# Kernel tuning notes

Hardware: AMD Instinct MI355X
Metric: run time of the kernel (lower is better)

## Reference

```python
import jax, jax.numpy as jnp
import numpy as np

L, B, H, D, P, T = 3, 64, 1024, 128, 64, 512  # layers, batch, hidden, input_dim, prompt, timesteps


def setup_inputs() -> dict:
    key = jax.random.key(0)
    ks = jax.random.split(key, 20)
    s = 1.0 / np.sqrt(H)  # PyTorch LSTM/Linear init scale
    u = lambda k, shape: jax.random.uniform(k, shape, jnp.float32, -s, s)
    inp = {
        "x": jax.random.uniform(ks[0], (P, B, D), jnp.float32),
        "h0": jax.random.normal(ks[1], (L, B, H), jnp.float32),
        "c0": jax.random.normal(ks[2], (L, B, H), jnp.float32),
        "W_ih0": u(ks[3], (4 * H, D)),
        "W_hh0": u(ks[4], (4 * H, H)),
        "b_ih0": u(ks[5], (4 * H,)),
        "b_hh0": u(ks[6], (4 * H,)),
        "W_ih1": u(ks[7], (4 * H, H)),
        "W_hh1": u(ks[8], (4 * H, H)),
        "b_ih1": u(ks[9], (4 * H,)),
        "b_hh1": u(ks[10], (4 * H,)),
        "W_ih2": u(ks[11], (4 * H, H)),
        "W_hh2": u(ks[12], (4 * H, H)),
        "b_ih2": u(ks[13], (4 * H,)),
        "b_hh2": u(ks[14], (4 * H,)),
        "W_fc": u(ks[15], (D, H)),
        "b_fc": u(ks[16], (D,)),
        "timesteps": T,
    }
    return inp


def _lstm_cell(inp, h, c, W_ih, W_hh, b):
    # PyTorch gate order: i, f, g, o
    gates = inp @ W_ih.T + h @ W_hh.T + b  # (B, 4H)
    i, f, g, o = jnp.split(gates, 4, axis=-1)
    c_new = jax.nn.sigmoid(f) * c + jax.nn.sigmoid(i) * jnp.tanh(g)
    h_new = jax.nn.sigmoid(o) * jnp.tanh(c_new)
    return h_new, c_new


def reference(x, h0, c0, W_ih0, W_hh0, b_ih0, b_hh0, W_ih1, W_hh1, b_ih1, b_hh1,
              W_ih2, W_hh2, b_ih2, b_hh2, W_fc, b_fc, timesteps):
    Tn = int(timesteps)
    Pn = x.shape[0]
    layers = [
        (W_ih0, W_hh0, b_ih0 + b_hh0),
        (W_ih1, W_hh1, b_ih1 + b_hh1),
        (W_ih2, W_hh2, b_ih2 + b_hh2),
    ]
    # teacher-forcing inputs padded to full horizon
    x_pad = jnp.zeros((Tn,) + x.shape[1:], x.dtype).at[:Pn].set(x)

    def step(carry, t):
        net_in, h, c = carry  # net_in (B,D); h,c (L,B,H)
        layer_in = net_in
        hs, cs = [], []
        for l, (Wi, Wh, b) in enumerate(layers):
            hl, cl = _lstm_cell(layer_in, h[l], c[l], Wi, Wh, b)
            hs.append(hl)
            cs.append(cl)
            layer_in = hl
        gen = jax.nn.sigmoid(layer_in @ W_fc.T + b_fc)  # (B, D)
        nxt = jnp.where(t + 1 < Pn, x_pad[t + 1], gen)
        return (nxt, jnp.stack(hs), jnp.stack(cs)), nxt

    init = (x[0], h0, c0)
    _, emitted = jax.lax.scan(step, init, jnp.arange(Tn - 1))  # (T-1, B, D)
    out = jnp.concatenate([x[:1], emitted], axis=0)  # (T, B, D)
    return out
```

## Files before the change

### kernel.cpp

```cpp
#include <hip/hip_runtime.h>

typedef short v8s __attribute__((ext_vector_type(8)));
typedef float f32x4 __attribute__((ext_vector_type(4)));
typedef unsigned short u16;

static constexpr int kB = 64;
static constexpr int kH = 1024;
static constexpr int kD = 128;
static constexpr int kL = 3;
static constexpr int NBLK = 128;
static constexpr int NTHR = 512;
static constexpr int NFLAG = 16384;

__device__ __forceinline__ u16 f2b(float f) {
  union { float f; unsigned u; } v; v.f = f;
  unsigned r = v.u + 0x7fffu + ((v.u >> 16) & 1u);
  return (u16)(r >> 16);
}

__device__ __forceinline__ float sigm(float x) { return 1.f / (1.f + expf(-x)); }

__device__ __forceinline__ void st16(u16* p, u16 v) {
  unsigned d = v;
  asm volatile("global_store_short %0, %1, off sc0 sc1" :: "v"(p), "v"(d) : "memory");
}
__device__ __forceinline__ void st32(float* p, float v) {
  asm volatile("global_store_dword %0, %1, off sc0 sc1" :: "v"(p), "v"(v) : "memory");
}
__device__ __forceinline__ void st32u(unsigned* p, unsigned v) {
  asm volatile("global_store_dword %0, %1, off sc0 sc1" :: "v"(p), "v"(v) : "memory");
}

__device__ __forceinline__ void ld4cv(v8s& a0, v8s& a1, v8s& a2, v8s& a3,
                                      const u16* p0, const u16* p1,
                                      const u16* p2, const u16* p3) {
  asm volatile(
      "global_load_dwordx4 %0, %4, off sc0 sc1\n\t"
      "global_load_dwordx4 %1, %5, off sc0 sc1\n\t"
      "global_load_dwordx4 %2, %6, off sc0 sc1\n\t"
      "global_load_dwordx4 %3, %7, off sc0 sc1"
      : "=&v"(a0), "=&v"(a1), "=&v"(a2), "=&v"(a3)
      : "v"(p0), "v"(p1), "v"(p2), "v"(p3)
      : "memory");
}
#define WAITV(N) do { asm volatile("s_waitcnt vmcnt(" #N ")" ::: "memory"); \
                      __builtin_amdgcn_sched_barrier(0); } while (0)
#define MFMA8(A, W, I, ACC) do { \
  _Pragma("unroll") \
  for (int mt_ = 0; mt_ < 4; ++mt_) { \
    ACC[0][mt_] = __builtin_amdgcn_mfma_f32_16x16x32_bf16(A[mt_], W[0][I], ACC[0][mt_], 0, 0, 0); \
    ACC[1][mt_] = __builtin_amdgcn_mfma_f32_16x16x32_bf16(A[mt_], W[1][I], ACC[1][mt_], 0, 0, 0); \
  } } while (0)

struct Params {
  const float *x, *h0, *c0;
  const float *Wi0, *Wh0, *bi0, *bh0;
  const float *Wi1, *Wh1, *bi1, *bh1;
  const float *Wi2, *Wh2, *bi2, *bh2;
  const float *Wfc, *bfc;
  float *out;
  u16 *wb0i, *wb0h, *wb1i, *wb1h, *wb2i, *wb2h, *wbfc;
  u16 *xb, *hA, *hB, *curx;
  float *b0, *b1, *b2, *bfcs;
  unsigned *bflags;
  int P, T;
};

__global__ void init_kernel(Params p) {
  long gid = (long)blockIdx.x * blockDim.x + threadIdx.x;
  long stride = (long)gridDim.x * blockDim.x;
  const long nw0i = 4096L * kD, nwh = 4096L * kH, nfc = (long)kD * kH;
  for (long i = gid; i < nw0i; i += stride) p.wb0i[i] = f2b(p.Wi0[i]);
  for (long i = gid; i < nwh; i += stride) {
    p.wb0h[i] = f2b(p.Wh0[i]);
    p.wb1i[i] = f2b(p.Wi1[i]);
    p.wb1h[i] = f2b(p.Wh1[i]);
    p.wb2i[i] = f2b(p.Wi2[i]);
    p.wb2h[i] = f2b(p.Wh2[i]);
  }
  for (long i = gid; i < nfc; i += stride) p.wbfc[i] = f2b(p.Wfc[i]);
  for (long i = gid; i < 4096; i += stride) {
    p.b0[i] = p.bi0[i] + p.bh0[i];
    p.b1[i] = p.bi1[i] + p.bh1[i];
    p.b2[i] = p.bi2[i] + p.bh2[i];
  }
  for (long i = gid; i < kD; i += stride) p.bfcs[i] = p.bfc[i];
  for (long i = gid; i < NFLAG; i += stride) p.bflags[i] = 0u;
  long nx = (long)p.P * kB * kD;
  for (long i = gid; i < nx; i += stride) {
    p.xb[i] = f2b(p.x[i]);
    p.out[i] = p.x[i];
  }
  long nh = (long)kL * kB * kH;
  for (long i = gid; i < nh; i += stride) p.hA[i] = f2b(p.h0[i]);
}

__global__ void __launch_bounds__(NTHR) rnn_kernel(Params p) {
  const int tid = threadIdx.x, bid = blockIdx.x;
  const int lane = tid & 63, w = tid >> 6;
  const int colc = lane & 15, kq = lane >> 4;
  const int aoff = kq * 8;
  const int u7 = colc & 7, gh = colc >> 3;
  const long wr0 = (long)gh * kH + bid * 8 + u7;
  const long wr1 = (long)(2 + gh) * kH + bid * 8 + u7;
  unsigned* f0arr = p.bflags;
  unsigned* f1arr = p.bflags + NBLK * 32;
  unsigned* f2arr = p.bflags + 2 * NBLK * 32;
  unsigned* xflag = p.bflags + 3 * NBLK * 32;

  v8s w0x[2];
  v8s w0h[2][4], w1x[2][4], w1h[2][4], w2x[2][4], w2h[2][4];
  if (w < 4) {
    w0x[0] = *(const v8s*)(p.wb0i + wr0 * kD + w * 32 + aoff);
    w0x[1] = *(const v8s*)(p.wb0i + wr1 * kD + w * 32 + aoff);
  }
#pragma unroll
  for (int i = 0; i < 4; ++i) {
    int k = (w + 8 * i) * 32 + aoff;
    w0h[0][i] = *(const v8s*)(p.wb0h + wr0 * kH + k);
    w0h[1][i] = *(const v8s*)(p.wb0h + wr1 * kH + k);
    w1x[0][i] = *(const v8s*)(p.wb1i + wr0 * kH + k);
    w1x[1][i] = *(const v8s*)(p.wb1i + wr1 * kH + k);
    w1h[0][i] = *(const v8s*)(p.wb1h + wr0 * kH + k);
    w1h[1][i] = *(const v8s*)(p.wb1h + wr1 * kH + k);
    w2x[0][i] = *(const v8s*)(p.wb2i + wr0 * kH + k);
    w2x[1][i] = *(const v8s*)(p.wb2i + wr1 * kH + k);
    w2h[0][i] = *(const v8s*)(p.wb2h + wr0 * kH + k);
    w2h[1][i] = *(const v8s*)(p.wb2h + wr1 * kH + k);
  }

  const int em = tid >> 3, eu = tid & 7;
  const int ehid = bid * 8 + eu;
  float cst[kL], brg[kL][4];
#pragma unroll
  for (int l = 0; l < kL; ++l)
    cst[l] = p.c0[(long)l * kB * kH + (long)em * kH + ehid];
  {
    const float* bp[3] = {p.b0, p.b1, p.b2};
#pragma unroll
    for (int l = 0; l < 3; ++l)
#pragma unroll
      for (int gg = 0; gg < 4; ++gg) brg[l][gg] = bp[l][gg * kH + ehid];
  }

  __shared__ float lg[8][64][18];
  const int T = p.T, P = p.P;
  const f32x4 z4 = {0.f, 0.f, 0.f, 0.f};

  auto epilogue = [&](int l, f32x4(&acc)[2][4], u16* hOut) {
    float pre[4];
#pragma unroll
    for (int mt = 0; mt < 4; ++mt)
#pragma unroll
      for (int r = 0; r < 4; ++r) lg[w][mt * 16 + kq * 4 + r][colc] = acc[0][mt][r];
    __syncthreads();
    {
      float s0 = 0.f, s1 = 0.f;
#pragma unroll
      for (int ww = 0; ww < 8; ++ww) {
        s0 += lg[ww][em][eu];
        s1 += lg[ww][em][8 + eu];
      }
      pre[0] = s0;
      pre[1] = s1;
    }
    __syncthreads();
#pragma unroll
    for (int mt = 0; mt < 4; ++mt)
#pragma unroll
      for (int r = 0; r < 4; ++r) lg[w][mt * 16 + kq * 4 + r][colc] = acc[1][mt][r];
    __syncthreads();
    {
      float s0 = 0.f, s1 = 0.f;
#pragma unroll
      for (int ww = 0; ww < 8; ++ww) {
        s0 += lg[ww][em][eu];
        s1 += lg[ww][em][8 + eu];
      }
      pre[2] = s0;
      pre[3] = s1;
    }
    float iv = pre[0] + brg[l][0], fv = pre[1] + brg[l][1];
    float gv = pre[2] + brg[l][2], ov = pre[3] + brg[l][3];
    float cn = sigm(fv) * cst[l] + sigm(iv) * tanhf(gv);
    cst[l] = cn;
    st16(hOut + (long)em * kH + ehid, f2b(sigm(ov) * tanhf(cn)));
  };

  auto arrive = [&](unsigned* farr, unsigned val) {
    asm volatile("s_waitcnt vmcnt(0)" ::: "memory");
    __syncthreads();
    if (tid == 0) st32u(farr + bid * 32, val);
  };

  auto poll16 = [&](unsigned* farr, unsigned tgt) {
    unsigned* fp = farr + (4 * (w + 8 * (lane >> 2)) + (lane & 3)) * 32;
    for (;;) {
      unsigned v = (lane < 16)
          ? __hip_atomic_load(fp, __ATOMIC_RELAXED, __HIP_MEMORY_SCOPE_AGENT)
          : tgt;
      if (__all((int)(v >= tgt))) break;
      __builtin_amdgcn_s_sleep(1);
    }
    asm volatile("" ::: "memory");
  };

  auto gemm16 = [&](const u16* Ab, v8s (&W)[2][4], f32x4 (&acc)[2][4]) {
    const u16* b0 = Ab + (long)colc * kH + w * 32 + aoff;
    const u16* b1 = b0 + 16 * kH;
    const u16* b2 = b0 + 32 * kH;
    const u16* b3 = b0 + 48 * kH;
    v8s A0[4], A1[4], A2[4], A3[4];
    ld4cv(A0[0], A0[1], A0[2], A0[3], b0, b1, b2, b3);
    ld4cv(A1[0], A1[1], A1[2], A1[3], b0 + 256, b1 + 256, b2 + 256, b3 + 256);
    WAITV(4);
    MFMA8(A0, W, 0, acc);
    ld4cv(A2[0], A2[1], A2[2], A2[3], b0 + 512, b1 + 512, b2 + 512, b3 + 512);
    WAITV(4);
    MFMA8(A1, W, 1, acc);
    ld4cv(A3[0], A3[1], A3[2], A3[3], b0 + 768, b1 + 768, b2 + 768, b3 + 768);
    WAITV(4);
    MFMA8(A2, W, 2, acc);
    WAITV(0);
    MFMA8(A3, W, 3, acc);
  };

  for (int t = 0; t < T - 1; ++t) {
    const u16* hOld = (t & 1) ? p.hB : p.hA;
    u16* hNew = (t & 1) ? p.hA : p.hB;
    const bool genstep = (t >= P);
    const unsigned ft = (unsigned)(t + 1);

    {
      f32x4 acc[2][4] = {z4, z4, z4, z4, z4, z4, z4, z4};
      if (genstep && bid < 8 && w < 4) {
        const unsigned t2 = (unsigned)t;
        unsigned* fa = f2arr + lane * 32;
        unsigned* fb = f2arr + (64 + lane) * 32;
        for (;;) {
          unsigned a = __hip_atomic_load(fa, __ATOMIC_RELAXED, __HIP_MEMORY_SCOPE_AGENT);
          unsigned b = __hip_atomic_load(fb, __ATOMIC_RELAXED, __HIP_MEMORY_SCOPE_AGENT);
          if (__all((int)((a >= t2) & (b >= t2)))) break;
          __builtin_amdgcn_s_sleep(1);
        }
        (void)__hip_atomic_load(f2arr, __ATOMIC_ACQUIRE, __HIP_MEMORY_SCOPE_AGENT);
        f32x4 u0 = z4, u1 = z4;
        const u16* ap = hOld + 2L * kB * kH + (long)(w * 16 + colc) * kH + aoff;
        const u16* bp = p.wbfc + (long)(bid * 16 + colc) * kH + aoff;
#pragma unroll
        for (int i = 0; i < 16; ++i) {
          v8s a0 = *(const v8s*)(ap + i * 32);
          v8s b0 = *(const v8s*)(bp + i * 32);
          v8s a1 = *(const v8s*)(ap + 512 + i * 32);
          v8s b1 = *(const v8s*)(bp + 512 + i * 32);
          u0 = __builtin_amdgcn_mfma_f32_16x16x32_bf16(a0, b0, u0, 0, 0, 0);
          u1 = __builtin_amdgcn_mfma_f32_16x16x32_bf16(a1, b1, u1, 0, 0, 0);
        }
        float bv = p.bfcs[bid * 16 + colc];
#pragma unroll
        for (int r = 0; r < 4; ++r) {
          float val = sigm(u0[r] + u1[r] + bv);
          int bb = w * 16 + kq * 4 + r, d = bid * 16 + colc;
          st32(p.out + (long)t * (kB * kD) + (long)bb * kD + d, val);
          st16(p.curx + (long)bb * kD + d, f2b(val));
        }
        asm volatile("s_waitcnt vmcnt(0)" ::: "memory");
        if (lane == 0)
          st32u(xflag + (bid * 4 + w) * 32, (unsigned)(t - P + 1));
      }
      gemm16(hOld, w0h, acc);
      if (w < 4) {
        if (genstep) {
          const unsigned tag = (unsigned)(t - P + 1);
          unsigned* fp = xflag + ((2 * w + (lane >> 2)) * 4 + (lane & 3)) * 32;
          for (;;) {
            unsigned v = (lane < 8)
                ? __hip_atomic_load(fp, __ATOMIC_RELAXED, __HIP_MEMORY_SCOPE_AGENT)
                : tag;
            if (__all((int)(v >= tag))) break;
            __builtin_amdgcn_s_sleep(1);
          }
          asm volatile("" ::: "memory");
          const u16* xb0 = p.curx + (long)colc * kD + w * 32 + aoff;
          v8s X[4];
          ld4cv(X[0], X[1], X[2], X[3],
                xb0, xb0 + 16 * kD, xb0 + 32 * kD, xb0 + 48 * kD);
          WAITV(0);
#pragma unroll
          for (int mt = 0; mt < 4; ++mt) {
            acc[0][mt] = __builtin_amdgcn_mfma_f32_16x16x32_bf16(X[mt], w0x[0], acc[0][mt], 0, 0, 0);
            acc[1][mt] = __builtin_amdgcn_mfma_f32_16x16x32_bf16(X[mt], w0x[1], acc[1][mt], 0, 0, 0);
          }
        } else {
          const u16* xin = p.xb + (long)t * kB * kD;
          int k = w * 32 + aoff;
#pragma unroll
          for (int mt = 0; mt < 4; ++mt) {
            v8s a = *(const v8s*)(xin + (long)(mt * 16 + colc) * kD + k);
            acc[0][mt] = __builtin_amdgcn_mfma_f32_16x16x32_bf16(a, w0x[0], acc[0][mt], 0, 0, 0);
            acc[1][mt] = __builtin_amdgcn_mfma_f32_16x16x32_bf16(a, w0x[1], acc[1][mt], 0, 0, 0);
          }
        }
      }
      epilogue(0, acc, hNew);
      arrive(f0arr, ft);
    }

    {
      f32x4 acc[2][4] = {z4, z4, z4, z4, z4, z4, z4, z4};
      gemm16(hOld + (long)kB * kH, w1h, acc);
      poll16(f0arr, ft);
      gemm16(hNew, w1x, acc);
      epilogue(1, acc, hNew + (long)kB * kH);
      arrive(f1arr, ft);
    }

    {
      f32x4 acc[2][4] = {z4, z4, z4, z4, z4, z4, z4, z4};
      gemm16(hOld + 2L * kB * kH, w2h, acc);
      poll16(f1arr, ft);
      gemm16(hNew + (long)kB * kH, w2x, acc);
      epilogue(2, acc, hNew + 2L * kB * kH);
      arrive(f2arr, ft);
    }
  }

  if (bid == 0 && T - 1 >= P && T >= 2) {
    const unsigned tgt = (unsigned)(T - 1);
    {
      const int i = threadIdx.x;
      unsigned* fp = f2arr + i * 32;
      for (;;) {
        unsigned v = (i < NBLK)
            ? __hip_atomic_load(fp, __ATOMIC_RELAXED, __HIP_MEMORY_SCOPE_AGENT)
            : tgt;
        if (__syncthreads_and((int)(v >= tgt))) break;
        __builtin_amdgcn_s_sleep(1);
      }
      if (tid == 0)
        (void)__hip_atomic_load(f2arr, __ATOMIC_ACQUIRE, __HIP_MEMORY_SCOPE_AGENT);
      __syncthreads();
    }
    const u16* hL = ((T - 2) & 1) ? p.hA : p.hB;
    const u16* wfc_r = p.wbfc + (long)(w * 16 + colc) * kH + aoff;
    const u16* ap = hL + 2L * kB * kH + (long)colc * kH + aoff;
    f32x4 fa[4] = {z4, z4, z4, z4};
#pragma unroll 2
    for (int kk = 0; kk < 32; ++kk) {
      v8s b = *(const v8s*)(wfc_r + kk * 32);
#pragma unroll
      for (int mt = 0; mt < 4; ++mt) {
        v8s a = *(const v8s*)(ap + mt * 16 * kH + kk * 32);
        fa[mt] = __builtin_amdgcn_mfma_f32_16x16x32_bf16(a, b, fa[mt], 0, 0, 0);
      }
    }
    float bv = p.bfcs[w * 16 + colc];
    float* orow = p.out + (long)(T - 1) * (kB * kD);
#pragma unroll
    for (int mt = 0; mt < 4; ++mt)
#pragma unroll
      for (int r = 0; r < 4; ++r) {
        int bb = mt * 16 + kq * 4 + r, d = w * 16 + colc;
        st32(orow + (long)bb * kD + d, sigm(fa[mt][r] + bv));
      }
  }
}

extern "C" void kernel_launch(void* const* d_in, const int* in_sizes, int n_in,
                              void* d_out, int out_size, void* d_ws, size_t ws_size,
                              hipStream_t stream) {
  Params p;
  p.x   = (const float*)d_in[0];
  p.h0  = (const float*)d_in[1];
  p.c0  = (const float*)d_in[2];
  p.Wi0 = (const float*)d_in[3];
  p.Wh0 = (const float*)d_in[4];
  p.bi0 = (const float*)d_in[5];
  p.bh0 = (const float*)d_in[6];
  p.Wi1 = (const float*)d_in[7];
  p.Wh1 = (const float*)d_in[8];
  p.bi1 = (const float*)d_in[9];
  p.bh1 = (const float*)d_in[10];
  p.Wi2 = (const float*)d_in[11];
  p.Wh2 = (const float*)d_in[12];
  p.bi2 = (const float*)d_in[13];
  p.bh2 = (const float*)d_in[14];
  p.Wfc = (const float*)d_in[15];
  p.bfc = (const float*)d_in[16];
  p.out = (float*)d_out;
  p.P = in_sizes[0] / (kB * kD);
  p.T = out_size / (kB * kD);

  char* w = (char*)d_ws;
  auto alloc = [&](size_t bytes) {
    char* r = w;
    w += (bytes + 255) & ~(size_t)255;
    return r;
  };
  p.wb0i = (u16*)alloc(4096L * kD * 2);
  p.wb0h = (u16*)alloc(4096L * kH * 2);
  p.wb1i = (u16*)alloc(4096L * kH * 2);
  p.wb1h = (u16*)alloc(4096L * kH * 2);
  p.wb2i = (u16*)alloc(4096L * kH * 2);
  p.wb2h = (u16*)alloc(4096L * kH * 2);
  p.wbfc = (u16*)alloc((long)kD * kH * 2);
  p.xb   = (u16*)alloc((long)p.P * kB * kD * 2);
  p.hA   = (u16*)alloc((long)kL * kB * kH * 2);
  p.hB   = (u16*)alloc((long)kL * kB * kH * 2);
  p.curx = (u16*)alloc((long)kB * kD * 2);
  p.b0   = (float*)alloc(4096 * 4);
  p.b1   = (float*)alloc(4096 * 4);
  p.b2   = (float*)alloc(4096 * 4);
  p.bfcs = (float*)alloc(kD * 4);
  p.bflags = (unsigned*)alloc(NFLAG * 4);

  hipLaunchKernelGGL(init_kernel, dim3(512), dim3(256), 0, stream, p);
  void* args[] = { &p };
  hipLaunchCooperativeKernel((const void*)rnn_kernel, dim3(NBLK), dim3(NTHR),
                             args, 0, stream);
}
```

Baseline: 19.54 ms.

## Offload FC head to dedicated blocks and merge epilogue LDS reductions

Adds eight extra cooperative blocks that compute only the output FC projection during generation steps, taking that work off the critical path of the first eight LSTM blocks. The FC blocks split the K dimension across two wave halves, reduce the halves through shared memory, and load their inputs with pipelined loads. The gate epilogue now stages both accumulator halves in one double-size LDS buffer, removing two barriers per layer. It also packs h outputs through LDS into 128-bit stores instead of scattered 16-bit stores. The launch bound now requests two blocks per CU, which could constrain register use for the register-resident weights.

```diff
diff --git a/kernel.cpp b/kernel.cpp
--- a/kernel.cpp
+++ b/kernel.cpp
@@ -9,6 +9,8 @@
 static constexpr int kD = 128;
 static constexpr int kL = 3;
 static constexpr int NBLK = 128;
+static constexpr int NFC = 8;
+static constexpr int NBLK_TOT = NBLK + NFC;
 static constexpr int NTHR = 512;
 static constexpr int NFLAG = 16384;
 
@@ -29,6 +31,9 @@
 }
 __device__ __forceinline__ void st32u(unsigned* p, unsigned v) {
   asm volatile("global_store_dword %0, %1, off sc0 sc1" :: "v"(p), "v"(v) : "memory");
+}
+__device__ __forceinline__ void st128(u16* p, v8s v) {
+  asm volatile("global_store_dwordx4 %0, %1, off sc0 sc1" :: "v"(p), "v"(v) : "memory");
 }
 
 __device__ __forceinline__ void ld4cv(v8s& a0, v8s& a1, v8s& a2, v8s& a3,
@@ -95,18 +100,85 @@
   for (long i = gid; i < nh; i += stride) p.hA[i] = f2b(p.h0[i]);
 }
 
-__global__ void __launch_bounds__(NTHR) rnn_kernel(Params p) {
+__global__ void __launch_bounds__(NTHR, 2) rnn_kernel(Params p) {
   const int tid = threadIdx.x, bid = blockIdx.x;
   const int lane = tid & 63, w = tid >> 6;
   const int colc = lane & 15, kq = lane >> 4;
   const int aoff = kq * 8;
-  const int u7 = colc & 7, gh = colc >> 3;
-  const long wr0 = (long)gh * kH + bid * 8 + u7;
-  const long wr1 = (long)(2 + gh) * kH + bid * 8 + u7;
   unsigned* f0arr = p.bflags;
   unsigned* f1arr = p.bflags + NBLK * 32;
   unsigned* f2arr = p.bflags + 2 * NBLK * 32;
   unsigned* xflag = p.bflags + 3 * NBLK * 32;
+  const int T = p.T, P = p.P;
+  const f32x4 z4 = {0.f, 0.f, 0.f, 0.f};
+
+  if (bid >= NBLK) {
+    if (T - 1 <= P) return;
+    __shared__ float fcred[4][64][4];
+    const int fbid = bid - NBLK;
+    const int wm = w & 3;
+    const int half = w >> 2;
+    const u16* bp = p.wbfc + (long)(fbid * 16 + colc) * kH + half * 512 + aoff;
+    const float bv = p.bfcs[fbid * 16 + colc];
+    for (int t = P; t < T - 1; ++t) {
+      const u16* hOld = (t & 1) ? p.hB : p.hA;
+      {
+        const unsigned tgt = (unsigned)t;
+        unsigned* fp = f2arr + (half * 64 + lane) * 32;
+        for (;;) {
+          unsigned v = __hip_atomic_load(fp, __ATOMIC_RELAXED, __HIP_MEMORY_SCOPE_AGENT);
+          if (__all((int)(v >= tgt))) break;
+          __builtin_amdgcn_s_sleep(1);
+        }
+        asm volatile("" ::: "memory");
+      }
+      const u16* ap = hOld + 2L * kB * kH + (long)(wm * 16 + colc) * kH + half * 512 + aoff;
+      f32x4 u = z4;
+      v8s A0[4], A1[4];
+      ld4cv(A0[0], A0[1], A0[2], A0[3], ap, ap + 32, ap + 64, ap + 96);
+      ld4cv(A1[0], A1[1], A1[2], A1[3], ap + 128, ap + 160, ap + 192, ap + 224);
+      WAITV(4);
+#pragma unroll
+      for (int j = 0; j < 4; ++j)
+        u = __builtin_amdgcn_mfma_f32_16x16x32_bf16(A0[j], *(const v8s*)(bp + j * 32), u, 0, 0, 0);
+      ld4cv(A0[0], A0[1], A0[2], A0[3], ap + 256, ap + 288, ap + 320, ap + 352);
+      WAITV(4);
+#pragma unroll
+      for (int j = 0; j < 4; ++j)
+        u = __builtin_amdgcn_mfma_f32_16x16x32_bf16(A1[j], *(const v8s*)(bp + (4 + j) * 32), u, 0, 0, 0);
+      ld4cv(A1[0], A1[1], A1[2], A1[3], ap + 384, ap + 416, ap + 448, ap + 480);
+      WAITV(4);
+#pragma unroll
+      for (int j = 0; j < 4; ++j)
+        u = __builtin_amdgcn_mfma_f32_16x16x32_bf16(A0[j], *(const v8s*)(bp + (8 + j) * 32), u, 0, 0, 0);
+      WAITV(0);
+#pragma unroll
+      for (int j = 0; j < 4; ++j)
+        u = __builtin_amdgcn_mfma_f32_16x16x32_bf16(A1[j], *(const v8s*)(bp + (12 + j) * 32), u, 0, 0, 0);
+      if (half) *(f32x4*)&fcred[wm][lane][0] = u;
+      __syncthreads();
+      if (!half) {
+        f32x4 up = *(const f32x4*)&fcred[wm][lane][0];
+        float* orow = p.out + (long)t * (kB * kD);
+#pragma unroll
+        for (int r = 0; r < 4; ++r) {
+          float val = sigm(u[r] + up[r] + bv);
+          int bb = wm * 16 + kq * 4 + r, d = fbid * 16 + colc;
+          st32(orow + (long)bb * kD + d, val);
+          st16(p.curx + (long)bb * kD + d, f2b(val));
+        }
+        asm volatile("s_waitcnt vmcnt(0)" ::: "memory");
+        if (lane == 0)
+          st32u(xflag + (fbid * 4 + wm) * 32, (unsigned)(t - P + 1));
+      }
+      __syncthreads();
+    }
+    return;
+  }
+
+  const int u7 = colc & 7, gh = colc >> 3;
+  const long wr0 = (long)gh * kH + bid * 8 + u7;
+  const long wr1 = (long)(2 + gh) * kH + bid * 8 + u7;
 
   v8s w0x[2];
   v8s w0h[2][4], w1x[2][4], w1h[2][4], w2x[2][4], w2h[2][4];
@@ -143,48 +215,36 @@
       for (int gg = 0; gg < 4; ++gg) brg[l][gg] = bp[l][gg * kH + ehid];
   }
 
-  __shared__ float lg[8][64][18];
-  const int T = p.T, P = p.P;
-  const f32x4 z4 = {0.f, 0.f, 0.f, 0.f};
+  __shared__ float lg[2][8][64][18];
+  __shared__ u16 hsh[8][64];
 
   auto epilogue = [&](int l, f32x4(&acc)[2][4], u16* hOut) {
-    float pre[4];
-#pragma unroll
-    for (int mt = 0; mt < 4; ++mt)
-#pragma unroll
-      for (int r = 0; r < 4; ++r) lg[w][mt * 16 + kq * 4 + r][colc] = acc[0][mt][r];
+#pragma unroll
+    for (int hh = 0; hh < 2; ++hh)
+#pragma unroll
+      for (int mt = 0; mt < 4; ++mt)
+#pragma unroll
+        for (int r = 0; r < 4; ++r)
+          lg[hh][w][mt * 16 + kq * 4 + r][colc] = acc[hh][mt][r];
     __syncthreads();
-    {
-      float s0 = 0.f, s1 = 0.f;
-#pragma unroll
-      for (int ww = 0; ww < 8; ++ww) {
-        s0 += lg[ww][em][eu];
-        s1 += lg[ww][em][8 + eu];
-      }
-      pre[0] = s0;
-      pre[1] = s1;
-    }
-    __syncthreads();
-#pragma unroll
-    for (int mt = 0; mt < 4; ++mt)
-#pragma unroll
-      for (int r = 0; r < 4; ++r) lg[w][mt * 16 + kq * 4 + r][colc] = acc[1][mt][r];
-    __syncthreads();
-    {
-      float s0 = 0.f, s1 = 0.f;
-#pragma unroll
-      for (int ww = 0; ww < 8; ++ww) {
-        s0 += lg[ww][em][eu];
-        s1 += lg[ww][em][8 + eu];
-      }
-      pre[2] = s0;
-      pre[3] = s1;
-    }
-    float iv = pre[0] + brg[l][0], fv = pre[1] + brg[l][1];
-    float gv = pre[2] + brg[l][2], ov = pre[3] + brg[l][3];
+    float s0 = 0.f, s1 = 0.f, s2 = 0.f, s3 = 0.f;
+#pragma unroll
+    for (int ww = 0; ww < 8; ++ww) {
+      s0 += lg[0][ww][em][eu];
+      s1 += lg[0][ww][em][8 + eu];
+      s2 += lg[1][ww][em][eu];
+      s3 += lg[1][ww][em][8 + eu];
+    }
+    float iv = s0 + brg[l][0], fv = s1 + brg[l][1];
+    float gv = s2 + brg[l][2], ov = s3 + brg[l][3];
     float cn = sigm(fv) * cst[l] + sigm(iv) * tanhf(gv);
     cst[l] = cn;
-    st16(hOut + (long)em * kH + ehid, f2b(sigm(ov) * tanhf(cn)));
+    hsh[w][lane] = f2b(sigm(ov) * tanhf(cn));
+    asm volatile("s_waitcnt lgkmcnt(0)" ::: "memory");
+    if (lane < 8) {
+      v8s hv = *(const v8s*)&hsh[w][lane * 8];
+      st128(hOut + (long)(w * 8 + lane) * kH + bid * 8, hv);
+    }
   };
 
   auto arrive = [&](unsigned* farr, unsigned val) {
@@ -233,41 +293,6 @@
 
     {
       f32x4 acc[2][4] = {z4, z4, z4, z4, z4, z4, z4, z4};
-      if (genstep && bid < 8 && w < 4) {
-        const unsigned t2 = (unsigned)t;
-        unsigned* fa = f2arr + lane * 32;
-        unsigned* fb = f2arr + (64 + lane) * 32;
-        for (;;) {
-          unsigned a = __hip_atomic_load(fa, __ATOMIC_RELAXED, __HIP_MEMORY_SCOPE_AGENT);
-          unsigned b = __hip_atomic_load(fb, __ATOMIC_RELAXED, __HIP_MEMORY_SCOPE_AGENT);
-          if (__all((int)((a >= t2) & (b >= t2)))) break;
-          __builtin_amdgcn_s_sleep(1);
-        }
-        (void)__hip_atomic_load(f2arr, __ATOMIC_ACQUIRE, __HIP_MEMORY_SCOPE_AGENT);
-        f32x4 u0 = z4, u1 = z4;
-        const u16* ap = hOld + 2L * kB * kH + (long)(w * 16 + colc) * kH + aoff;
-        const u16* bp = p.wbfc + (long)(bid * 16 + colc) * kH + aoff;
-#pragma unroll
-        for (int i = 0; i < 16; ++i) {
-          v8s a0 = *(const v8s*)(ap + i * 32);
-          v8s b0 = *(const v8s*)(bp + i * 32);
-          v8s a1 = *(const v8s*)(ap + 512 + i * 32);
-          v8s b1 = *(const v8s*)(bp + 512 + i * 32);
-          u0 = __builtin_amdgcn_mfma_f32_16x16x32_bf16(a0, b0, u0, 0, 0, 0);
-          u1 = __builtin_amdgcn_mfma_f32_16x16x32_bf16(a1, b1, u1, 0, 0, 0);
-        }
-        float bv = p.bfcs[bid * 16 + colc];
-#pragma unroll
-        for (int r = 0; r < 4; ++r) {
-          float val = sigm(u0[r] + u1[r] + bv);
-          int bb = w * 16 + kq * 4 + r, d = bid * 16 + colc;
-          st32(p.out + (long)t * (kB * kD) + (long)bb * kD + d, val);
-          st16(p.curx + (long)bb * kD + d, f2b(val));
-        }
-        asm volatile("s_waitcnt vmcnt(0)" ::: "memory");
-        if (lane == 0)
-          st32u(xflag + (bid * 4 + w) * 32, (unsigned)(t - P + 1));
-      }
       gemm16(hOld, w0h, acc);
       if (w < 4) {
         if (genstep) {
@@ -416,6 +441,6 @@
 
   hipLaunchKernelGGL(init_kernel, dim3(512), dim3(256), 0, stream, p);
   void* args[] = { &p };
-  hipLaunchCooperativeKernel((const void*)rnn_kernel, dim3(NBLK), dim3(NTHR),
+  hipLaunchCooperativeKernel((const void*)rnn_kernel, dim3(NBLK_TOT), dim3(NTHR),
                              args, 0, stream);
 }
```

Measured after the change: 17.11 ms. 1.14x faster.
